# Optimization experiments

Measured on AMD Instinct MI355X. Metric: run time of the kernel, lower is better.

Reference implementation:

```python
import jax, jax.numpy as jnp
import numpy as np

B, N, H = 8, 1024, 768
NH, HD = 12, 64  # num heads, head size
E = 131072       # total edges (avg degree 16)
N_REL = 30


def setup_inputs() -> dict:
    key = jax.random.key(0)
    ks = jax.random.split(key, 8)
    node_states = jax.random.normal(ks[0], (B, N, H), dtype=jnp.float32)
    eb = jax.random.randint(ks[1], (E,), 0, B, dtype=jnp.int32)
    ei = jax.random.randint(ks[2], (E,), 0, N, dtype=jnp.int32)
    ej = jax.random.randint(ks[3], (E,), 0, N, dtype=jnp.int32)
    er = jax.random.randint(ks[4], (E,), 0, N_REL, dtype=jnp.int32)
    edge_indices = jnp.stack([eb, ei, ej, er], axis=0)  # (4, E)
    scale = 1.0 / np.sqrt(H)
    Wq = jax.random.normal(ks[5], (H, H), dtype=jnp.float32) * scale
    Wk = jax.random.normal(ks[6], (H, H), dtype=jnp.float32) * scale
    Wv = jax.random.normal(ks[7], (H, H), dtype=jnp.float32) * scale
    return {"node_states": node_states, "edge_indices": edge_indices,
            "Wq": Wq, "Wk": Wk, "Wv": Wv}


def reference(node_states, edge_indices, Wq, Wk, Wv):
    # node_states: (B, N, H); edge_indices: (4, E) rows = (batch, head_node, tail_node, relation)
    b, i, j = edge_indices[0], edge_indices[1], edge_indices[2]
    q = (node_states @ Wq).reshape(B, N, NH, HD)
    k = (node_states @ Wk).reshape(B, N, NH, HD)
    v = (node_states @ Wv).reshape(B, N, NH, HD)
    qe = q[b, i]  # (E, NH, HD) gather at head nodes
    ke = k[b, j]  # (E, NH, HD) gather at tail nodes
    scores = jnp.einsum('ehd,ehd->eh', qe, ke) * (1.0 / np.sqrt(HD))  # (E, NH)
    seg = b * N + i  # segment = (batch, head_node)
    nseg = B * N
    smax = jax.ops.segment_max(scores, seg, num_segments=nseg)  # (nseg, NH)
    ex = jnp.exp(scores - smax[seg])
    denom = jax.ops.segment_sum(ex, seg, num_segments=nseg)
    probs = ex / jnp.maximum(denom[seg], 1e-9)  # (E, NH) edge softmax over tail nodes
    ve = v[b, j]  # (E, NH, HD)
    out_e = (probs[:, :, None] * ve).reshape(E, NH * HD)
    out = jax.ops.segment_sum(out_e, seg, num_segments=nseg)  # sum over tail dim
    return out.reshape(B, N, H)
```

## Files before the change

### kernel.cpp

```cpp
#include <hip/hip_runtime.h>

#define BB 8
#define NN 1024
#define HH 768
#define NHEAD 12
#define HD 64
#define NSEG 8192
#define QKVN 2304
#define MAXDEG 64

typedef unsigned short u16;
typedef __attribute__((ext_vector_type(8))) short bf16x8;
typedef __attribute__((ext_vector_type(4))) float f32x4;

__device__ __forceinline__ float bf2f(u16 v) {
  return __uint_as_float(((unsigned)v) << 16);
}
__device__ __forceinline__ u16 f2bf(float f) {
  unsigned u = __float_as_uint(f);
  u += 0x7FFFu + ((u >> 16) & 1u);
  return (u16)(u >> 16);
}

__global__ void cast_x_kernel(const float* __restrict__ X, u16* __restrict__ Xb) {
  int i = blockIdx.x * blockDim.x + threadIdx.x;
  float4 f = ((const float4*)X)[i];
  ushort4 o;
  o.x = f2bf(f.x); o.y = f2bf(f.y); o.z = f2bf(f.z); o.w = f2bf(f.w);
  ((ushort4*)Xb)[i] = o;
}

__global__ void transpose_w_kernel(const float* __restrict__ Wq,
                                   const float* __restrict__ Wk,
                                   const float* __restrict__ Wv,
                                   u16* __restrict__ Wt) {
  __shared__ float tile[32][33];
  int n0 = blockIdx.x * 32;
  int k0 = blockIdx.y * 32;
  const float* W = (n0 < HH) ? Wq : (n0 < 2 * HH ? Wk : Wv);
  int nb = n0 - (n0 < HH ? 0 : (n0 < 2 * HH ? HH : 2 * HH));
  int tx = threadIdx.x, ty = threadIdx.y;
#pragma unroll
  for (int r = 0; r < 4; ++r)
    tile[ty + 8 * r][tx] = W[(k0 + ty + 8 * r) * HH + nb + tx];
  __syncthreads();
#pragma unroll
  for (int r = 0; r < 4; ++r)
    Wt[(n0 + ty + 8 * r) * HH + k0 + tx] = f2bf(tile[tx][ty + 8 * r]);
}

__global__ void build_kernel(const int* __restrict__ EI, int* __restrict__ cursor,
                             int* __restrict__ tailrow, int E) {
  int e = blockIdx.x * blockDim.x + threadIdx.x;
  if (e >= E) return;
  int b = EI[e];
  int seg = b * NN + EI[E + e];
  int j = EI[2 * E + e];
  int pos = atomicAdd(&cursor[seg], 1);
  if (pos < MAXDEG) tailrow[seg * MAXDEG + pos] = b * NN + j;
}

#define BM 128
#define BN 128
#define BK 32

__global__ __launch_bounds__(256) void gemm_kernel(const u16* __restrict__ Xb,
                                                   const u16* __restrict__ Wt,
                                                   u16* __restrict__ QKV) {
  __shared__ u16 As[BM * BK];
  __shared__ u16 Bs[BN * BK];
  const int tid = threadIdx.x;
  const int wave = tid >> 6;
  const int lane = tid & 63;
  const int m0 = blockIdx.y * BM;
  const int n0 = blockIdx.x * BN;
  const int wr = wave >> 1;
  const int wc = wave & 1;
  const int quad = lane >> 4;
  const int l15 = lane & 15;

  f32x4 acc[4][4] = {};

  const int srow = wave * 16 + (lane >> 2);
  const int scol = (lane & 3) * 8;

  for (int kt = 0; kt < HH; kt += BK) {
    __syncthreads();
#pragma unroll
    for (int p = 0; p < 2; ++p) {
      const u16* ga = Xb + (m0 + p * 64 + srow) * HH + kt + scol;
      const u16* gb = Wt + (n0 + p * 64 + srow) * HH + kt + scol;
      u16* la = As + p * 2048 + wave * 512;
      u16* lb = Bs + p * 2048 + wave * 512;
      __builtin_amdgcn_global_load_lds(
          (const __attribute__((address_space(1))) unsigned int*)(unsigned long long)ga,
          (__attribute__((address_space(3))) unsigned int*)(unsigned long long)la, 16, 0, 0);
      __builtin_amdgcn_global_load_lds(
          (const __attribute__((address_space(1))) unsigned int*)(unsigned long long)gb,
          (__attribute__((address_space(3))) unsigned int*)(unsigned long long)lb, 16, 0, 0);
    }
    __syncthreads();

    bf16x8 afr[4], bfr[4];
#pragma unroll
    for (int mi = 0; mi < 4; ++mi)
      afr[mi] = *(const bf16x8*)(As + (wr * 64 + mi * 16 + l15) * BK + quad * 8);
#pragma unroll
    for (int ni = 0; ni < 4; ++ni)
      bfr[ni] = *(const bf16x8*)(Bs + (wc * 64 + ni * 16 + l15) * BK + quad * 8);
#pragma unroll
    for (int mi = 0; mi < 4; ++mi)
#pragma unroll
      for (int ni = 0; ni < 4; ++ni)
        acc[mi][ni] = __builtin_amdgcn_mfma_f32_16x16x32_bf16(afr[mi], bfr[ni], acc[mi][ni], 0, 0, 0);
  }

#pragma unroll
  for (int mi = 0; mi < 4; ++mi)
#pragma unroll
    for (int ni = 0; ni < 4; ++ni) {
      int col = n0 + wc * 64 + ni * 16 + l15;
#pragma unroll
      for (int r = 0; r < 4; ++r) {
        int row = m0 + wr * 64 + mi * 16 + quad * 4 + r;
        QKV[row * QKVN + col] = f2bf(acc[mi][ni][r]);
      }
    }
}

__global__ __launch_bounds__(256) void attn_kernel(const u16* __restrict__ QKV,
                                                   const int* __restrict__ tailrow,
                                                   const int* __restrict__ cursor,
                                                   float* __restrict__ out) {
  const int seg = blockIdx.x * 4 + (threadIdx.x >> 6);
  const int lane = threadIdx.x & 63;
  const int base = seg * MAXDEG;
  int cnt = cursor[seg];
  if (cnt > MAXDEG) cnt = MAXDEG;

  const u16* qrow = QKV + seg * QKVN;
  float qv1[8], qv2[4];
  {
    bf16x8 q1 = *(const bf16x8*)(qrow + lane * 8);
    ushort4 q2 = *(const ushort4*)(qrow + 512 + lane * 4);
#pragma unroll
    for (int i = 0; i < 8; ++i) qv1[i] = bf2f((u16)q1[i]) * 0.125f;
    qv2[0] = bf2f(q2.x) * 0.125f; qv2[1] = bf2f(q2.y) * 0.125f;
    qv2[2] = bf2f(q2.z) * 0.125f; qv2[3] = bf2f(q2.w) * 0.125f;
  }

  float mA1 = -__builtin_inff(), lA1 = 0.f, mA2 = -__builtin_inff(), lA2 = 0.f;
  float mB1 = -__builtin_inff(), lB1 = 0.f, mB2 = -__builtin_inff(), lB2 = 0.f;
  float oA1[8] = {}, oA2[4] = {}, oB1[8] = {}, oB2[4] = {};

  auto loadkv = [&](int row, bf16x8& k1, ushort4& k2, bf16x8& v1, ushort4& v2) {
    const u16* kp = QKV + row * QKVN + HH;
    k1 = *(const bf16x8*)(kp + lane * 8);
    k2 = *(const ushort4*)(kp + 512 + lane * 4);
    v1 = *(const bf16x8*)(kp + HH + lane * 8);
    v2 = *(const ushort4*)(kp + HH + 512 + lane * 4);
  };

  auto process = [&](bf16x8 k1, ushort4 k2, bf16x8 v1, ushort4 v2,
                     float& m1, float& l1, float* o1,
                     float& m2, float& l2, float* o2) {
    float s1 = 0.f;
#pragma unroll
    for (int i = 0; i < 8; ++i) s1 += qv1[i] * bf2f((u16)k1[i]);
    s1 += __shfl_xor(s1, 1, 64);
    s1 += __shfl_xor(s1, 2, 64);
    s1 += __shfl_xor(s1, 4, 64);
    float s2 = qv2[0] * bf2f(k2.x) + qv2[1] * bf2f(k2.y) +
               qv2[2] * bf2f(k2.z) + qv2[3] * bf2f(k2.w);
    s2 += __shfl_xor(s2, 1, 64);
    s2 += __shfl_xor(s2, 2, 64);
    s2 += __shfl_xor(s2, 4, 64);
    s2 += __shfl_xor(s2, 8, 64);
    {
      float mn = fmaxf(m1, s1);
      float al = __expf(m1 - mn);
      float ex = __expf(s1 - mn);
      l1 = l1 * al + ex;
#pragma unroll
      for (int i = 0; i < 8; ++i) o1[i] = o1[i] * al + ex * bf2f((u16)v1[i]);
      m1 = mn;
    }
    {
      float mn = fmaxf(m2, s2);
      float al = __expf(m2 - mn);
      float ex = __expf(s2 - mn);
      l2 = l2 * al + ex;
      o2[0] = o2[0] * al + ex * bf2f(v2.x);
      o2[1] = o2[1] * al + ex * bf2f(v2.y);
      o2[2] = o2[2] * al + ex * bf2f(v2.z);
      o2[3] = o2[3] * al + ex * bf2f(v2.w);
      m2 = mn;
    }
  };

  if (cnt >= 2) {
    bf16x8 k1A, v1A, k1B, v1B, nk1A, nv1A, nk1B, nv1B;
    ushort4 k2A, v2A, k2B, v2B, nk2A, nv2A, nk2B, nv2B;
    loadkv(tailrow[base], k1A, k2A, v1A, v2A);
    loadkv(tailrow[base + 1], k1B, k2B, v1B, v2B);
    const int npair = cnt >> 1;
    for (int p = 0; p < npair; ++p) {
      int i2 = 2 * p + 2;
      int ia = (i2 < cnt) ? i2 : 0;
      int ib = (i2 + 1 < cnt) ? i2 + 1 : ia;
      loadkv(tailrow[base + ia], nk1A, nk2A, nv1A, nv2A);
      loadkv(tailrow[base + ib], nk1B, nk2B, nv1B, nv2B);
      process(k1A, k2A, v1A, v2A, mA1, lA1, oA1, mA2, lA2, oA2);
      process(k1B, k2B, v1B, v2B, mB1, lB1, oB1, mB2, lB2, oB2);
      k1A = nk1A; k2A = nk2A; v1A = nv1A; v2A = nv2A;
      k1B = nk1B; k2B = nk2B; v1B = nv1B; v2B = nv2B;
    }
    if (cnt & 1)
      process(k1A, k2A, v1A, v2A, mA1, lA1, oA1, mA2, lA2, oA2);
  } else if (cnt == 1) {
    bf16x8 k1A, v1A; ushort4 k2A, v2A;
    loadkv(tailrow[base], k1A, k2A, v1A, v2A);
    process(k1A, k2A, v1A, v2A, mA1, lA1, oA1, mA2, lA2, oA2);
  }

  float res1[8], res2[4];
  {
    float mn = fmaxf(fmaxf(mA1, mB1), -1e30f);
    float aA = __expf(mA1 - mn), aB = __expf(mB1 - mn);
    float l = lA1 * aA + lB1 * aB;
    float inv = 1.f / fmaxf(l, 1e-9f);
#pragma unroll
    for (int i = 0; i < 8; ++i) res1[i] = (oA1[i] * aA + oB1[i] * aB) * inv;
  }
  {
    float mn = fmaxf(fmaxf(mA2, mB2), -1e30f);
    float aA = __expf(mA2 - mn), aB = __expf(mB2 - mn);
    float l = lA2 * aA + lB2 * aB;
    float inv = 1.f / fmaxf(l, 1e-9f);
#pragma unroll
    for (int i = 0; i < 4; ++i) res2[i] = (oA2[i] * aA + oB2[i] * aB) * inv;
  }

  float* op = out + seg * HH;
  float4 r0 = {res1[0], res1[1], res1[2], res1[3]};
  float4 r1 = {res1[4], res1[5], res1[6], res1[7]};
  float4 r2 = {res2[0], res2[1], res2[2], res2[3]};
  ((float4*)(op + lane * 8))[0] = r0;
  ((float4*)(op + lane * 8))[1] = r1;
  *(float4*)(op + 512 + lane * 4) = r2;
}

extern "C" void kernel_launch(void* const* d_in, const int* in_sizes, int n_in,
                              void* d_out, int out_size, void* d_ws, size_t ws_size,
                              hipStream_t stream) {
  const float* X  = (const float*)d_in[0];
  const int*   EI = (const int*)d_in[1];
  const float* Wq = (const float*)d_in[2];
  const float* Wk = (const float*)d_in[3];
  const float* Wv = (const float*)d_in[4];
  float* out = (float*)d_out;
  const int E = in_sizes[1] / 4;

  char* ws = (char*)d_ws;
  int* cursor  = (int*)(ws);
  int* tailrow = (int*)(ws + 32768);
  u16* Xb      = (u16*)(ws + 2129920);
  u16* Wt      = (u16*)(ws + 14712832);
  u16* QKV     = (u16*)(ws + 18251776);

  hipMemsetAsync(cursor, 0, NSEG * 4, stream);

  cast_x_kernel<<<(NSEG * HH / 4) / 256, 256, 0, stream>>>(X, Xb);
  transpose_w_kernel<<<dim3(QKVN / 32, HH / 32), dim3(32, 8), 0, stream>>>(Wq, Wk, Wv, Wt);
  build_kernel<<<(E + 255) / 256, 256, 0, stream>>>(EI, cursor, tailrow, E);
  gemm_kernel<<<dim3(QKVN / BN, NSEG / BM), 256, 0, stream>>>(Xb, Wt, QKV);
  attn_kernel<<<NSEG / 4, 256, 0, stream>>>(QKV, tailrow, cursor, out);
}
```

Baseline: 206.1 us.

## Split each segment's edges across two wavefronts and merge softmax state via LDS

The attention kernel now gives each segment two wavefronts instead of one. Each wavefront runs an online softmax over alternating edges, and the two partial states (max, sum, accumulators) are combined through shared memory after a block barrier. The aim is more memory-level parallelism and shorter serial dependency chains per segment on the gather-bound edge loop. In exchange it doubles the block count, adds an LDS round-trip and a __syncthreads, and leaves half the waves idle during the final write.

```diff
diff --git a/kernel.cpp b/kernel.cpp
--- a/kernel.cpp
+++ b/kernel.cpp
@@ -132,11 +132,16 @@
                                                    const int* __restrict__ tailrow,
                                                    const int* __restrict__ cursor,
                                                    float* __restrict__ out) {
-  const int seg = blockIdx.x * 4 + (threadIdx.x >> 6);
+  __shared__ float sm[2 * 16 * 64];
+  const int wv = threadIdx.x >> 6;
   const int lane = threadIdx.x & 63;
+  const int sIb = wv >> 1;
+  const int half = wv & 1;
+  const int seg = blockIdx.x * 2 + sIb;
   const int base = seg * MAXDEG;
   int cnt = cursor[seg];
   if (cnt > MAXDEG) cnt = MAXDEG;
+  const int myn = (cnt > half) ? ((cnt - half + 1) >> 1) : 0;
 
   const u16* qrow = QKV + seg * QKVN;
   float qv1[8], qv2[4];
@@ -149,9 +154,9 @@
     qv2[2] = bf2f(q2.z) * 0.125f; qv2[3] = bf2f(q2.w) * 0.125f;
   }
 
-  float mA1 = -__builtin_inff(), lA1 = 0.f, mA2 = -__builtin_inff(), lA2 = 0.f;
-  float mB1 = -__builtin_inff(), lB1 = 0.f, mB2 = -__builtin_inff(), lB2 = 0.f;
-  float oA1[8] = {}, oA2[4] = {}, oB1[8] = {}, oB2[4] = {};
+  float m1 = -__builtin_inff(), l1 = 0.f;
+  float m2 = -__builtin_inff(), l2 = 0.f;
+  float o1[8] = {}, o2[4] = {};
 
   auto loadkv = [&](int row, bf16x8& k1, ushort4& k2, bf16x8& v1, ushort4& v2) {
     const u16* kp = QKV + row * QKVN + HH;
@@ -161,93 +166,93 @@
     v2 = *(const ushort4*)(kp + HH + 512 + lane * 4);
   };
 
-  auto process = [&](bf16x8 k1, ushort4 k2, bf16x8 v1, ushort4 v2,
-                     float& m1, float& l1, float* o1,
-                     float& m2, float& l2, float* o2) {
-    float s1 = 0.f;
-#pragma unroll
-    for (int i = 0; i < 8; ++i) s1 += qv1[i] * bf2f((u16)k1[i]);
-    s1 += __shfl_xor(s1, 1, 64);
-    s1 += __shfl_xor(s1, 2, 64);
-    s1 += __shfl_xor(s1, 4, 64);
-    float s2 = qv2[0] * bf2f(k2.x) + qv2[1] * bf2f(k2.y) +
-               qv2[2] * bf2f(k2.z) + qv2[3] * bf2f(k2.w);
-    s2 += __shfl_xor(s2, 1, 64);
-    s2 += __shfl_xor(s2, 2, 64);
-    s2 += __shfl_xor(s2, 4, 64);
-    s2 += __shfl_xor(s2, 8, 64);
+  if (myn > 0) {
+    bf16x8 k1, v1, k1n, v1n;
+    ushort4 k2, v2, k2n, v2n;
+    loadkv(tailrow[base + half], k1, k2, v1, v2);
+    for (int t = 0; t < myn; ++t) {
+      int tn = (t + 1 < myn) ? t + 1 : t;
+      loadkv(tailrow[base + half + 2 * tn], k1n, k2n, v1n, v2n);
+
+      float s1 = 0.f;
+#pragma unroll
+      for (int i = 0; i < 8; ++i) s1 += qv1[i] * bf2f((u16)k1[i]);
+      s1 += __shfl_xor(s1, 1, 64);
+      s1 += __shfl_xor(s1, 2, 64);
+      s1 += __shfl_xor(s1, 4, 64);
+      float s2 = qv2[0] * bf2f(k2.x) + qv2[1] * bf2f(k2.y) +
+                 qv2[2] * bf2f(k2.z) + qv2[3] * bf2f(k2.w);
+      s2 += __shfl_xor(s2, 1, 64);
+      s2 += __shfl_xor(s2, 2, 64);
+      s2 += __shfl_xor(s2, 4, 64);
+      s2 += __shfl_xor(s2, 8, 64);
+
+      {
+        float mn = fmaxf(m1, s1);
+        float al = __expf(m1 - mn);
+        float ex = __expf(s1 - mn);
+        l1 = l1 * al + ex;
+#pragma unroll
+        for (int i = 0; i < 8; ++i) o1[i] = o1[i] * al + ex * bf2f((u16)v1[i]);
+        m1 = mn;
+      }
+      {
+        float mn = fmaxf(m2, s2);
+        float al = __expf(m2 - mn);
+        float ex = __expf(s2 - mn);
+        l2 = l2 * al + ex;
+        o2[0] = o2[0] * al + ex * bf2f(v2.x);
+        o2[1] = o2[1] * al + ex * bf2f(v2.y);
+        o2[2] = o2[2] * al + ex * bf2f(v2.z);
+        o2[3] = o2[3] * al + ex * bf2f(v2.w);
+        m2 = mn;
+      }
+      k1 = k1n; k2 = k2n; v1 = v1n; v2 = v2n;
+    }
+  }
+
+  float* sb = sm + sIb * 16 * 64;
+  if (half == 1) {
+    sb[0 * 64 + lane] = m1;  sb[1 * 64 + lane] = l1;
+    sb[2 * 64 + lane] = m2;  sb[3 * 64 + lane] = l2;
+#pragma unroll
+    for (int i = 0; i < 8; ++i) sb[(4 + i) * 64 + lane] = o1[i];
+#pragma unroll
+    for (int i = 0; i < 4; ++i) sb[(12 + i) * 64 + lane] = o2[i];
+  }
+  __syncthreads();
+  if (half == 0) {
+    float mB1 = sb[0 * 64 + lane], lB1 = sb[1 * 64 + lane];
+    float mB2 = sb[2 * 64 + lane], lB2 = sb[3 * 64 + lane];
+
+    float res1[8], res2[4];
     {
-      float mn = fmaxf(m1, s1);
-      float al = __expf(m1 - mn);
-      float ex = __expf(s1 - mn);
-      l1 = l1 * al + ex;
-#pragma unroll
-      for (int i = 0; i < 8; ++i) o1[i] = o1[i] * al + ex * bf2f((u16)v1[i]);
-      m1 = mn;
+      float mn = fmaxf(fmaxf(m1, mB1), -1e30f);
+      float aA = __expf(m1 - mn), aB = __expf(mB1 - mn);
+      float l = l1 * aA + lB1 * aB;
+      float inv = 1.f / fmaxf(l, 1e-9f);
+#pragma unroll
+      for (int i = 0; i < 8; ++i)
+        res1[i] = (o1[i] * aA + sb[(4 + i) * 64 + lane] * aB) * inv;
     }
     {
-      float mn = fmaxf(m2, s2);
-      float al = __expf(m2 - mn);
-      float ex = __expf(s2 - mn);
-      l2 = l2 * al + ex;
-      o2[0] = o2[0] * al + ex * bf2f(v2.x);
-      o2[1] = o2[1] * al + ex * bf2f(v2.y);
-      o2[2] = o2[2] * al + ex * bf2f(v2.z);
-      o2[3] = o2[3] * al + ex * bf2f(v2.w);
-      m2 = mn;
-    }
-  };
-
-  if (cnt >= 2) {
-    bf16x8 k1A, v1A, k1B, v1B, nk1A, nv1A, nk1B, nv1B;
-    ushort4 k2A, v2A, k2B, v2B, nk2A, nv2A, nk2B, nv2B;
-    loadkv(tailrow[base], k1A, k2A, v1A, v2A);
-    loadkv(tailrow[base + 1], k1B, k2B, v1B, v2B);
-    const int npair = cnt >> 1;
-    for (int p = 0; p < npair; ++p) {
-      int i2 = 2 * p + 2;
-      int ia = (i2 < cnt) ? i2 : 0;
-      int ib = (i2 + 1 < cnt) ? i2 + 1 : ia;
-      loadkv(tailrow[base + ia], nk1A, nk2A, nv1A, nv2A);
-      loadkv(tailrow[base + ib], nk1B, nk2B, nv1B, nv2B);
-      process(k1A, k2A, v1A, v2A, mA1, lA1, oA1, mA2, lA2, oA2);
-      process(k1B, k2B, v1B, v2B, mB1, lB1, oB1, mB2, lB2, oB2);
-      k1A = nk1A; k2A = nk2A; v1A = nv1A; v2A = nv2A;
-      k1B = nk1B; k2B = nk2B; v1B = nv1B; v2B = nv2B;
-    }
-    if (cnt & 1)
-      process(k1A, k2A, v1A, v2A, mA1, lA1, oA1, mA2, lA2, oA2);
-  } else if (cnt == 1) {
-    bf16x8 k1A, v1A; ushort4 k2A, v2A;
-    loadkv(tailrow[base], k1A, k2A, v1A, v2A);
-    process(k1A, k2A, v1A, v2A, mA1, lA1, oA1, mA2, lA2, oA2);
-  }
-
-  float res1[8], res2[4];
-  {
-    float mn = fmaxf(fmaxf(mA1, mB1), -1e30f);
-    float aA = __expf(mA1 - mn), aB = __expf(mB1 - mn);
-    float l = lA1 * aA + lB1 * aB;
-    float inv = 1.f / fmaxf(l, 1e-9f);
-#pragma unroll
-    for (int i = 0; i < 8; ++i) res1[i] = (oA1[i] * aA + oB1[i] * aB) * inv;
-  }
-  {
-    float mn = fmaxf(fmaxf(mA2, mB2), -1e30f);
-    float aA = __expf(mA2 - mn), aB = __expf(mB2 - mn);
-    float l = lA2 * aA + lB2 * aB;
-    float inv = 1.f / fmaxf(l, 1e-9f);
-#pragma unroll
-    for (int i = 0; i < 4; ++i) res2[i] = (oA2[i] * aA + oB2[i] * aB) * inv;
-  }
-
-  float* op = out + seg * HH;
-  float4 r0 = {res1[0], res1[1], res1[2], res1[3]};
-  float4 r1 = {res1[4], res1[5], res1[6], res1[7]};
-  float4 r2 = {res2[0], res2[1], res2[2], res2[3]};
-  ((float4*)(op + lane * 8))[0] = r0;
-  ((float4*)(op + lane * 8))[1] = r1;
-  *(float4*)(op + 512 + lane * 4) = r2;
+      float mn = fmaxf(fmaxf(m2, mB2), -1e30f);
+      float aA = __expf(m2 - mn), aB = __expf(mB2 - mn);
+      float l = l2 * aA + lB2 * aB;
+      float inv = 1.f / fmaxf(l, 1e-9f);
+#pragma unroll
+      for (int i = 0; i < 4; ++i)
+        res2[i] = (o2[i] * aA + sb[(12 + i) * 64 + lane] * aB) * inv;
+    }
+
+    float* op = out + seg * HH;
+    float4 r0 = {res1[0], res1[1], res1[2], res1[3]};
+    float4 r1 = {res1[4], res1[5], res1[6], res1[7]};
+    float4 r2 = {res2[0], res2[1], res2[2], res2[3]};
+    ((float4*)(op + lane * 8))[0] = r0;
+    ((float4*)(op + lane * 8))[1] = r1;
+    *(float4*)(op + 512 + lane * 4) = r2;
+  }
 }
 
 extern "C" void kernel_launch(void* const* d_in, const int* in_sizes, int n_in,
@@ -274,5 +279,5 @@
   transpose_w_kernel<<<dim3(QKVN / 32, HH / 32), dim3(32, 8), 0, stream>>>(Wq, Wk, Wv, Wt);
   build_kernel<<<(E + 255) / 256, 256, 0, stream>>>(EI, cursor, tailrow, E);
   gemm_kernel<<<dim3(QKVN / BN, NSEG / BM), 256, 0, stream>>>(Xb, Wt, QKV);
-  attn_kernel<<<NSEG / 4, 256, 0, stream>>>(QKV, tailrow, cursor, out);
-}
+  attn_kernel<<<NSEG / 2, 256, 0, stream>>>(QKV, tailrow, cursor, out);
+}
```

After: 191.5 us. 1.08x faster.
